# Optimization experiments

Measured on AMD Instinct MI355X. Metric: run time of the kernel, lower is better.

## Reference

```python
import jax, jax.numpy as jnp
import numpy as np

B, S, D, H, E, K = 4, 2048, 1024, 2048, 8, 2
MU, GAMMA, LN_EPS = 0.7, 1.0, 1e-5


def setup_inputs() -> dict:
    key = jax.random.key(0)
    ks = jax.random.split(key, 8)
    inv_d = 1.0 / np.sqrt(D)
    inv_h = 1.0 / np.sqrt(H)
    return {
        "x": jax.random.normal(ks[0], (B, S, D), dtype=jnp.float32),
        "momentum": jax.random.normal(ks[1], (B, S, D), dtype=jnp.float32),
        "Wg": jax.random.normal(ks[2], (D, E), dtype=jnp.float32) * inv_d,
        "bg": jnp.zeros((E,), dtype=jnp.float32),
        "W1": jax.random.normal(ks[3], (E, D, H), dtype=jnp.float32) * inv_d,
        "b1": jnp.zeros((E, H), dtype=jnp.float32),
        "W2": jax.random.normal(ks[4], (E, H, D), dtype=jnp.float32) * inv_h,
        "b2": jnp.zeros((E, D), dtype=jnp.float32),
        "ln_g": jnp.ones((D,), dtype=jnp.float32),
        "ln_b": jnp.zeros((D,), dtype=jnp.float32),
    }


def reference(x, momentum, Wg, bg, W1, b1, W2, b2, ln_g, ln_b):
    # --- TopKGate: linear router, softmax over top-k logits, zeros elsewhere ---
    logits = jnp.einsum("bsd,de->bse", x, Wg) + bg            # [B,S,E]
    top_v, top_i = jax.lax.top_k(logits, K)                    # [B,S,K]
    top_w = jax.nn.softmax(top_v, axis=-1)                     # [B,S,K]
    gates = jnp.sum(jax.nn.one_hot(top_i, E, dtype=x.dtype) * top_w[..., None], axis=-2)  # [B,S,E]

    # --- Dense all-expert FFN (faithful to the original per-expert loop) ---
    h = jax.nn.relu(jnp.einsum("bsd,edh->bseh", x, W1) + b1)   # [B,S,E,H]
    eo = jnp.einsum("bseh,ehd->bsed", h, W2) + b2              # [B,S,E,D]
    expert_outputs = jnp.einsum("bse,bsed->bsd", gates, eo)    # [B,S,D]

    # --- Momentum update + residual + LayerNorm ---
    new_momentum = -expert_outputs + MU * momentum
    out = x + GAMMA * new_momentum
    mean = jnp.mean(out, axis=-1, keepdims=True)
    var = jnp.mean(jnp.square(out - mean), axis=-1, keepdims=True)
    out = (out - mean) * jax.lax.rsqrt(var + LN_EPS) * ln_g + ln_b
    return out, new_momentum
```

## Files before the change

### kernel.cpp

```cpp
#include <hip/hip_runtime.h>

#define TT 8192
#define DD 1024
#define HHH 2048
#define EE 8
#define MUf 0.7f
#define GAMMAf 1.0f
#define LNEPS 1e-5f

typedef __bf16 bf16x8 __attribute__((ext_vector_type(8)));
typedef float floatx4 __attribute__((ext_vector_type(4)));

__device__ __forceinline__ unsigned short f2bf(float f) {
  unsigned u = __float_as_uint(f);
  u += 0x7FFFu + ((u >> 16) & 1u);
  return (unsigned short)(u >> 16);
}
__device__ __forceinline__ float bf2f(unsigned short u) {
  return __uint_as_float(((unsigned)u) << 16);
}
__device__ __forceinline__ void load_lds16(const void* g, void* l) {
  __builtin_amdgcn_global_load_lds(
      (__attribute__((address_space(1))) void*)g,
      (__attribute__((address_space(3))) void*)l,
      16, 0, 0);
}

__global__ __launch_bounds__(256) void cvt_router_kernel(
    const float* __restrict__ x, const float* __restrict__ Wg, const float* __restrict__ bg,
    unsigned short* __restrict__ xb,
    int* __restrict__ pair_e, float* __restrict__ pair_w) {
  int tid = threadIdx.x;
  size_t gi = (size_t)blockIdx.x * 2048 + (size_t)tid * 8;
  const float4* s = (const float4*)(x + gi);
  float4 a = s[0], b = s[1];
  unsigned r0 = f2bf(a.x) | ((unsigned)f2bf(a.y) << 16);
  unsigned r1 = f2bf(a.z) | ((unsigned)f2bf(a.w) << 16);
  unsigned r2 = f2bf(b.x) | ((unsigned)f2bf(b.y) << 16);
  unsigned r3 = f2bf(b.z) | ((unsigned)f2bf(b.w) << 16);
  ((uint4*)xb)[blockIdx.x * 256 + tid] = make_uint4(r0, r1, r2, r3);

  float xa[8] = {a.x, a.y, a.z, a.w, b.x, b.y, b.z, b.w};
  int d0 = (tid & 127) * 8;
  const float* wbase = Wg + (size_t)d0 * EE;
  float acc[EE];
#pragma unroll
  for (int e = 0; e < EE; ++e) acc[e] = 0.f;
#pragma unroll
  for (int i = 0; i < 8; ++i) {
    float4 w0 = *(const float4*)(wbase + i * EE);
    float4 w1 = *(const float4*)(wbase + i * EE + 4);
    acc[0] += xa[i] * w0.x; acc[1] += xa[i] * w0.y;
    acc[2] += xa[i] * w0.z; acc[3] += xa[i] * w0.w;
    acc[4] += xa[i] * w1.x; acc[5] += xa[i] * w1.y;
    acc[6] += xa[i] * w1.z; acc[7] += xa[i] * w1.w;
  }
#pragma unroll
  for (int e = 0; e < EE; ++e) {
#pragma unroll
    for (int off = 32; off > 0; off >>= 1) acc[e] += __shfl_xor(acc[e], off);
  }
  __shared__ float rs[4][EE];
  int wv = tid >> 6;
  if ((tid & 63) == 0) {
#pragma unroll
    for (int e = 0; e < EE; ++e) rs[wv][e] = acc[e];
  }
  __syncthreads();
  if ((tid & 127) == 0) {
    int half = tid >> 7;
    int t = blockIdx.x * 2 + half;
    float v[EE];
#pragma unroll
    for (int e = 0; e < EE; ++e) v[e] = rs[2 * half][e] + rs[2 * half + 1][e] + bg[e];
    int i0 = 0;
#pragma unroll
    for (int e = 1; e < EE; ++e) if (v[e] > v[i0]) i0 = e;
    int i1 = (i0 == 0) ? 1 : 0;
#pragma unroll
    for (int e = 0; e < EE; ++e) if (e != i0 && v[e] > v[i1]) i1 = e;
    float w1e = __expf(v[i1] - v[i0]);
    float inv = 1.f / (1.f + w1e);
    pair_e[2 * t] = i0;     pair_w[2 * t] = inv;
    pair_e[2 * t + 1] = i1; pair_w[2 * t + 1] = w1e * inv;
  }
}

__global__ __launch_bounds__(256) void count_kernel(const int* __restrict__ pair_e,
                                                    int* __restrict__ counts) {
  __shared__ int lh[EE];
  int tid = threadIdx.x;
  if (tid < EE) lh[tid] = 0;
  __syncthreads();
  int p = blockIdx.x * 256 + tid;
  atomicAdd(&lh[pair_e[p]], 1);
  __syncthreads();
  if (tid < EE) atomicAdd(&counts[tid], lh[tid]);
}

__global__ void prefix_kernel(const int* __restrict__ counts, int* __restrict__ offs,
                              int* __restrict__ cursor) {
  if (threadIdx.x == 0) {
    int s = 0;
    for (int e = 0; e < EE; ++e) { offs[e] = s; cursor[e] = s; s += counts[e]; }
    offs[EE] = s;
  }
}

__global__ __launch_bounds__(256) void scatter_kernel(const int* __restrict__ pair_e,
                                                      int* __restrict__ cursor,
                                                      int* __restrict__ pair_rows) {
  __shared__ int lh[EE];
  __shared__ int lb[EE];
  int tid = threadIdx.x;
  if (tid < EE) lh[tid] = 0;
  __syncthreads();
  int p = blockIdx.x * 256 + tid;
  int e = pair_e[p];
  int r = atomicAdd(&lh[e], 1);
  __syncthreads();
  if (tid < EE) lb[tid] = atomicAdd(&cursor[tid], lh[tid]);
  __syncthreads();
  pair_rows[lb[e] + r] = p;
}

__global__ __launch_bounds__(256) void transpose_cvt_kernel(
    const float* __restrict__ w1, unsigned short* __restrict__ o1,
    const float* __restrict__ w2, unsigned short* __restrict__ o2) {
  __shared__ float tile[64][65];
  int bid = blockIdx.x;
  int half = bid >> 12;
  int e = (bid >> 9) & 7;
  int tl = bid & 511;
  int R, C, tx, ty;
  const float* src;
  unsigned short* dst;
  if (half == 0) {
    R = DD; C = HHH; tx = tl & 31; ty = tl >> 5;
    src = w1 + (size_t)e * R * C; dst = o1 + (size_t)e * R * C;
  } else {
    R = HHH; C = DD; tx = tl & 15; ty = tl >> 4;
    src = w2 + (size_t)e * R * C; dst = o2 + (size_t)e * R * C;
  }
  int c0 = tx * 64, r0 = ty * 64;
  int t = threadIdx.x;
  int q = t & 15, r = t >> 4;
#pragma unroll
  for (int i = 0; i < 4; ++i) {
    int rr = r + 16 * i;
    float4 v = *(const float4*)(src + (size_t)(r0 + rr) * C + c0 + q * 4);
    tile[rr][q * 4 + 0] = v.x; tile[rr][q * 4 + 1] = v.y;
    tile[rr][q * 4 + 2] = v.z; tile[rr][q * 4 + 3] = v.w;
  }
  __syncthreads();
  int g = t & 15, cc = t >> 4;
#pragma unroll
  for (int i = 0; i < 4; ++i) {
    int c = cc + 16 * i;
    ushort4 o;
    o.x = f2bf(tile[g * 4 + 0][c]);
    o.y = f2bf(tile[g * 4 + 1][c]);
    o.z = f2bf(tile[g * 4 + 2][c]);
    o.w = f2bf(tile[g * 4 + 3][c]);
    *(ushort4*)(dst + (size_t)(c0 + c) * R + r0 + g * 4) = o;
  }
}

template <int MODE>
__global__ __launch_bounds__(256, 3) void moe_gemm_kernel(
    const unsigned short* __restrict__ Amat, const unsigned short* __restrict__ Bmat,
    const float* __restrict__ bias, const int* __restrict__ offsets,
    const int* __restrict__ pair_rows, const float* __restrict__ pair_w,
    unsigned short* __restrict__ Out, int Kd, int Nd, int nxlog) {
  int d = blockIdx.x;
  int e = d & 7;
  int lin = d >> 3;
  int mt0 = lin >> nxlog;
  int n0 = (lin & ((1 << nxlog) - 1)) << 7;
  int off = offsets[e];
  int cnt = offsets[e + 1] - off;
  int tid = threadIdx.x;
  int lane = tid & 63, wid = tid >> 6;

  __shared__ unsigned short As[3][128 * 32];
  __shared__ unsigned short Bs[3][128 * 32];

  const unsigned short* Bex = Bmat + (size_t)e * Nd * Kd;
  int csw = (((tid & 3) ^ ((tid >> 2) & 3)) * 8);
  int wm = (wid >> 1) * 64, wn = (wid & 1) * 64;
  int lr = lane & 15;
  int t4 = lane >> 4;
  int lka = ((t4 ^ (lr & 3)) * 8);
  int NT = Kd >> 5;

  for (int mt = mt0; mt * 128 < cnt; mt += 32) {
    __syncthreads();

    const unsigned short* aptr[2];
    const unsigned short* bptr[2];
#pragma unroll
    for (int P = 0; P < 2; ++P) {
      int row = P * 64 + (tid >> 2);
      int sa = mt * 128 + row;
      if (sa >= cnt) sa = cnt - 1;
      int gr = (MODE == 0) ? (pair_rows[off + sa] >> 1) : (off + sa);
      aptr[P] = Amat + (size_t)gr * Kd + csw;
      bptr[P] = Bex + (size_t)(n0 + row) * Kd + csw;
    }

    floatx4 acc[4][4];
#pragma unroll
    for (int m = 0; m < 4; ++m)
#pragma unroll
      for (int n = 0; n < 4; ++n) acc[m][n] = (floatx4){0.f, 0.f, 0.f, 0.f};

#pragma unroll
    for (int P = 0; P < 2; ++P) {
      load_lds16(aptr[P], &As[0][P * 2048] + tid * 8);
      load_lds16(bptr[P], &Bs[0][P * 2048] + tid * 8);
    }
#pragma unroll
    for (int P = 0; P < 2; ++P) {
      load_lds16(aptr[P] + 32, &As[1][P * 2048] + tid * 8);
      load_lds16(bptr[P] + 32, &Bs[1][P * 2048] + tid * 8);
    }

    for (int kt = 0; kt < NT; ++kt) {
      if (kt + 1 < NT) {
        asm volatile("s_waitcnt vmcnt(4)" ::: "memory");
      } else {
        asm volatile("s_waitcnt vmcnt(0)" ::: "memory");
      }
      __builtin_amdgcn_s_barrier();
      __builtin_amdgcn_sched_barrier(0);
      int pf = kt + 2;
      if (pf < NT) {
        int ko = pf * 32;
        int pb = pf - (pf / 3) * 3;
#pragma unroll
        for (int P = 0; P < 2; ++P) {
          load_lds16(aptr[P] + ko, &As[pb][P * 2048] + tid * 8);
          load_lds16(bptr[P] + ko, &Bs[pb][P * 2048] + tid * 8);
        }
      }
      int b = kt - (kt / 3) * 3;
      bf16x8 af[4], bfr[4];
#pragma unroll
      for (int m = 0; m < 4; ++m)
        af[m] = *(const bf16x8*)(&As[b][(wm + m * 16 + lr) * 32 + lka]);
#pragma unroll
      for (int n = 0; n < 4; ++n)
        bfr[n] = *(const bf16x8*)(&Bs[b][(wn + n * 16 + lr) * 32 + lka]);
#pragma unroll
      for (int m = 0; m < 4; ++m)
#pragma unroll
        for (int n = 0; n < 4; ++n)
          acc[m][n] = __builtin_amdgcn_mfma_f32_16x16x32_bf16(af[m], bfr[n], acc[m][n], 0, 0, 0);
    }

    int rem = cnt - mt * 128;
    if (rem > 128) rem = 128;
#pragma unroll
    for (int m = 0; m < 4; ++m) {
#pragma unroll
      for (int j = 0; j < 4; ++j) {
        int lrr = wm + m * 16 + ((lane >> 4) << 2) + j;
        if (lrr < rem) {
          int s = mt * 128 + lrr;
          size_t orow;
          float scale = 1.f;
          if (MODE == 0) {
            orow = (size_t)(off + s) * Nd;
          } else {
            int p = pair_rows[off + s];
            orow = (size_t)p * Nd;
            scale = pair_w[p];
          }
#pragma unroll
          for (int n = 0; n < 4; ++n) {
            int col = n0 + wn + n * 16 + lr;
            float v = acc[m][n][j] + bias[e * Nd + col];
            if (MODE == 0) v = fmaxf(v, 0.f);
            else v *= scale;
            Out[orow + col] = f2bf(v);
          }
        }
      }
    }
  }
}

__global__ __launch_bounds__(256) void final_kernel(
    const float* __restrict__ x, const float* __restrict__ mom,
    const unsigned short* __restrict__ pairout, const float* __restrict__ ln_g,
    const float* __restrict__ ln_b, float* __restrict__ outp, float* __restrict__ nmp) {
  int t = blockIdx.x, tid = threadIdx.x;
  int d0 = tid * 4;
  size_t rowoff = (size_t)t * DD;
  const unsigned short* p0 = pairout + (size_t)(2 * t) * DD;
  const unsigned short* p1 = p0 + DD;
  float4 xv = *(const float4*)(x + rowoff + d0);
  float4 mv = *(const float4*)(mom + rowoff + d0);
  ushort4 u0 = *(const ushort4*)(p0 + d0);
  ushort4 u1 = *(const ushort4*)(p1 + d0);
  float eo[4] = {bf2f(u0.x) + bf2f(u1.x), bf2f(u0.y) + bf2f(u1.y),
                 bf2f(u0.z) + bf2f(u1.z), bf2f(u0.w) + bf2f(u1.w)};
  float xa[4] = {xv.x, xv.y, xv.z, xv.w};
  float ma[4] = {mv.x, mv.y, mv.z, mv.w};
  float o[4], nm[4];
  float s1 = 0.f, s2 = 0.f;
#pragma unroll
  for (int j = 0; j < 4; ++j) {
    nm[j] = MUf * ma[j] - eo[j];
    o[j] = xa[j] + GAMMAf * nm[j];
    s1 += o[j];
    s2 += o[j] * o[j];
  }
  *(float4*)(nmp + rowoff + d0) = make_float4(nm[0], nm[1], nm[2], nm[3]);
#pragma unroll
  for (int off = 32; off > 0; off >>= 1) {
    s1 += __shfl_xor(s1, off);
    s2 += __shfl_xor(s2, off);
  }
  __shared__ float rs[8];
  int wid = tid >> 6, lane = tid & 63;
  if (lane == 0) { rs[wid] = s1; rs[4 + wid] = s2; }
  __syncthreads();
  s1 = rs[0] + rs[1] + rs[2] + rs[3];
  s2 = rs[4] + rs[5] + rs[6] + rs[7];
  float mean = s1 * (1.f / DD);
  float var = s2 * (1.f / DD) - mean * mean;
  float rstd = rsqrtf(var + LNEPS);
  float4 g = *(const float4*)(ln_g + d0);
  float4 bb = *(const float4*)(ln_b + d0);
  float ga[4] = {g.x, g.y, g.z, g.w}, ba[4] = {bb.x, bb.y, bb.z, bb.w};
  float res[4];
#pragma unroll
  for (int j = 0; j < 4; ++j) res[j] = (o[j] - mean) * rstd * ga[j] + ba[j];
  *(float4*)(outp + rowoff + d0) = make_float4(res[0], res[1], res[2], res[3]);
}

extern "C" void kernel_launch(void* const* d_in, const int* in_sizes, int n_in,
                              void* d_out, int out_size, void* d_ws, size_t ws_size,
                              hipStream_t stream) {
  const float* x   = (const float*)d_in[0];
  const float* mom = (const float*)d_in[1];
  const float* Wg  = (const float*)d_in[2];
  const float* bg  = (const float*)d_in[3];
  const float* W1  = (const float*)d_in[4];
  const float* b1  = (const float*)d_in[5];
  const float* W2  = (const float*)d_in[6];
  const float* b2  = (const float*)d_in[7];
  const float* lng = (const float*)d_in[8];
  const float* lnb = (const float*)d_in[9];
  (void)in_sizes; (void)n_in; (void)out_size; (void)ws_size;
  float* outp = (float*)d_out;
  float* nmp  = outp + (size_t)TT * DD;

  char* base = (char*)d_ws;
  size_t off = 0;
  auto carve = [&](size_t bytes) {
    void* p = base + off;
    off += (bytes + 255) & ~(size_t)255;
    return p;
  };
  unsigned short* xb   = (unsigned short*)carve((size_t)TT * DD * 2);
  unsigned short* w1t  = (unsigned short*)carve((size_t)EE * HHH * DD * 2);
  unsigned short* w2t  = (unsigned short*)carve((size_t)EE * DD * HHH * 2);
  unsigned short* hbuf = (unsigned short*)carve((size_t)2 * TT * HHH * 2);
  unsigned short* pout = (unsigned short*)carve((size_t)2 * TT * DD * 2);
  int*   pair_e    = (int*)carve((size_t)2 * TT * 4);
  float* pair_w    = (float*)carve((size_t)2 * TT * 4);
  int*   pair_rows = (int*)carve((size_t)2 * TT * 4);
  int*   counts    = (int*)carve(256);
  int*   offs      = (int*)carve(256);
  int*   cursor    = (int*)carve(256);

  hipMemsetAsync(counts, 0, EE * sizeof(int), stream);
  cvt_router_kernel<<<TT / 2, 256, 0, stream>>>(x, Wg, bg, xb, pair_e, pair_w);
  count_kernel<<<(2 * TT) / 256, 256, 0, stream>>>(pair_e, counts);
  prefix_kernel<<<1, 64, 0, stream>>>(counts, offs, cursor);
  scatter_kernel<<<(2 * TT) / 256, 256, 0, stream>>>(pair_e, cursor, pair_rows);
  transpose_cvt_kernel<<<8192, 256, 0, stream>>>(W1, w1t, W2, w2t);
  moe_gemm_kernel<0><<<EE * (HHH / 128) * 32, 256, 0, stream>>>(
      xb, w1t, b1, offs, pair_rows, pair_w, hbuf, DD, HHH, 4);
  moe_gemm_kernel<1><<<EE * (DD / 128) * 32, 256, 0, stream>>>(
      hbuf, w2t, b2, offs, pair_rows, pair_w, pout, HHH, DD, 3);
  final_kernel<<<TT, 256, 0, stream>>>(x, mom, pout, lng, lnb, outp, nmp);
}
```

Measured before the change: 317.7 us.

## Unroll GEMM k-loop by two with paired prefetch into triple-buffered LDS

Restructures the grouped-GEMM main loop to handle two k-tiles per iteration. It waits for all outstanding loads once, computes the first tile, then issues prefetches for the next two tiles into the freed buffers before computing the second tile. The aim is fewer waitcnt and barrier sync points and simpler buffer-index arithmetic. In exchange it uses a full vmcnt(0) wait, so each prefetch has only one tile of compute to hide its latency, and it assumes an even tile count.

```diff
diff --git a/kernel.cpp b/kernel.cpp
--- a/kernel.cpp
+++ b/kernel.cpp
@@ -225,38 +225,60 @@
       load_lds16(bptr[P] + 32, &Bs[1][P * 2048] + tid * 8);
     }
 
-    for (int kt = 0; kt < NT; ++kt) {
-      if (kt + 1 < NT) {
-        asm volatile("s_waitcnt vmcnt(4)" ::: "memory");
-      } else {
-        asm volatile("s_waitcnt vmcnt(0)" ::: "memory");
+    int s0 = 0;
+    int NP = NT >> 1;
+    for (int P = 0; P < NP; ++P) {
+      int kt = 2 * P;
+      int sB = s0 + 1; if (sB == 3) sB = 0;
+      int tg0 = s0 + 2; if (tg0 >= 3) tg0 -= 3;
+      asm volatile("s_waitcnt vmcnt(0)" ::: "memory");
+      __builtin_amdgcn_s_barrier();
+      {
+        bf16x8 af[4], bfr[4];
+#pragma unroll
+        for (int m = 0; m < 4; ++m)
+          af[m] = *(const bf16x8*)(&As[s0][(wm + m * 16 + lr) * 32 + lka]);
+#pragma unroll
+        for (int n = 0; n < 4; ++n)
+          bfr[n] = *(const bf16x8*)(&Bs[s0][(wn + n * 16 + lr) * 32 + lka]);
+#pragma unroll
+        for (int m = 0; m < 4; ++m)
+#pragma unroll
+          for (int n = 0; n < 4; ++n)
+            acc[m][n] = __builtin_amdgcn_mfma_f32_16x16x32_bf16(af[m], bfr[n], acc[m][n], 0, 0, 0);
       }
       __builtin_amdgcn_s_barrier();
       __builtin_amdgcn_sched_barrier(0);
-      int pf = kt + 2;
-      if (pf < NT) {
-        int ko = pf * 32;
-        int pb = pf - (pf / 3) * 3;
-#pragma unroll
-        for (int P = 0; P < 2; ++P) {
-          load_lds16(aptr[P] + ko, &As[pb][P * 2048] + tid * 8);
-          load_lds16(bptr[P] + ko, &Bs[pb][P * 2048] + tid * 8);
+      if (kt + 2 < NT) {
+        int ko2 = (kt + 2) * 32, ko3 = (kt + 3) * 32;
+#pragma unroll
+        for (int Q = 0; Q < 2; ++Q) {
+          load_lds16(aptr[Q] + ko2, &As[tg0][Q * 2048] + tid * 8);
+          load_lds16(bptr[Q] + ko2, &Bs[tg0][Q * 2048] + tid * 8);
+        }
+#pragma unroll
+        for (int Q = 0; Q < 2; ++Q) {
+          load_lds16(aptr[Q] + ko3, &As[s0][Q * 2048] + tid * 8);
+          load_lds16(bptr[Q] + ko3, &Bs[s0][Q * 2048] + tid * 8);
         }
       }
-      int b = kt - (kt / 3) * 3;
-      bf16x8 af[4], bfr[4];
-#pragma unroll
-      for (int m = 0; m < 4; ++m)
-        af[m] = *(const bf16x8*)(&As[b][(wm + m * 16 + lr) * 32 + lka]);
-#pragma unroll
-      for (int n = 0; n < 4; ++n)
-        bfr[n] = *(const bf16x8*)(&Bs[b][(wn + n * 16 + lr) * 32 + lka]);
-#pragma unroll
-      for (int m = 0; m < 4; ++m)
+      {
+        bf16x8 af[4], bfr[4];
+#pragma unroll
+        for (int m = 0; m < 4; ++m)
+          af[m] = *(const bf16x8*)(&As[sB][(wm + m * 16 + lr) * 32 + lka]);
 #pragma unroll
         for (int n = 0; n < 4; ++n)
-          acc[m][n] = __builtin_amdgcn_mfma_f32_16x16x32_bf16(af[m], bfr[n], acc[m][n], 0, 0, 0);
+          bfr[n] = *(const bf16x8*)(&Bs[sB][(wn + n * 16 + lr) * 32 + lka]);
+#pragma unroll
+        for (int m = 0; m < 4; ++m)
+#pragma unroll
+          for (int n = 0; n < 4; ++n)
+            acc[m][n] = __builtin_amdgcn_mfma_f32_16x16x32_bf16(af[m], bfr[n], acc[m][n], 0, 0, 0);
+      }
+      s0 = tg0;
     }
+    asm volatile("s_waitcnt vmcnt(0)" ::: "memory");
 
     int rem = cnt - mt * 128;
     if (rem > 128) rem = 128;
```

New measurement: 300.2 us (median of 2 runs). -5.5%, faster.
